# Kernel tuning notes

Measured on AMD Instinct MI355X. Metric: run time of the kernel, lower is better.

Reference implementation:

```python
import jax, jax.numpy as jnp
import numpy as np

C_IN, C_OUT, N, H, W = 128, 256, 3, 256, 256


def im2row(x, n, h, w, c):
    """x: [h*w, c] channel-last pixel-major image -> [(h-n+1)*(w-n+1), c*n*n]
    with each row ordered (channel, ki, kj) to match w.reshape(C_OUT,-1).T."""
    img = x.reshape(h, w, c)
    oh, ow = h - n + 1, w - n + 1
    # stack the n*n shifted views; last axis index = ki*n + kj
    patches = jnp.stack(
        [img[ki:ki + oh, kj:kj + ow, :] for ki in range(n) for kj in range(n)],
        axis=-1,
    )  # [oh, ow, c, n*n]
    return patches.reshape(oh * ow, c * n * n)


def setup_inputs() -> dict:
    key = jax.random.key(0)
    k1, k2, k3, k4 = jax.random.split(key, 4)
    x = jax.random.normal(k1, (H * W, C_IN), dtype=jnp.float32)
    # pre-quantized int8 kernel values (stored as int32), symmetric range
    kernel_q = jax.random.randint(k2, (C_IN * N * N, C_OUT), -127, 128, dtype=jnp.int32)
    kernel_scale = jax.random.uniform(k3, (1,), dtype=jnp.float32, minval=1e-3, maxval=1e-2)
    bias = jax.random.normal(k4, (C_OUT,), dtype=jnp.float32)
    return {"x": x, "kernel_q": kernel_q, "kernel_scale": kernel_scale, "bias": bias}


def reference(x, kernel_q, kernel_scale, bias):
    # im2row unfolding (irregular gather)
    rows = im2row(x, N, H, W, C_IN)                      # [OH*OW, C_IN*N*N]
    # int8 quantized matmul (weights dequantized by per-tensor scale) + bias
    acc = rows @ kernel_q.astype(jnp.float32)            # [OH*OW, C_OUT]
    return acc * kernel_scale + bias
```

## Files before the change

### kernel.cpp

```cpp
#include <hip/hip_runtime.h>
#include <hip/hip_bf16.h>
#include <stdint.h>

#define HH 256
#define WW 256
#define CIN 128
#define COUT 256
#define OHW 64516
#define KTOT 1152

#define BM 128
#define BN 256
#define BK 64
#define NSTEP 18

typedef __attribute__((ext_vector_type(8))) short short8;
typedef __attribute__((ext_vector_type(4))) float float4v;
typedef __attribute__((ext_vector_type(4))) float f32x4;

__device__ __forceinline__ short f2bf(float f) {
    unsigned u = __builtin_bit_cast(unsigned, f);
    unsigned r = u + 0x7fffu + ((u >> 16) & 1u);
    return (short)(r >> 16);
}

__device__ __forceinline__ short8 cvt8(float4v a, float4v b) {
    short8 r;
    r[0] = f2bf(a[0]); r[1] = f2bf(a[1]); r[2] = f2bf(a[2]); r[3] = f2bf(a[3]);
    r[4] = f2bf(b[0]); r[5] = f2bf(b[1]); r[6] = f2bf(b[2]); r[7] = f2bf(b[3]);
    return r;
}

__global__ void prep_weights(const int* __restrict__ kq, unsigned short* __restrict__ wt) {
    int tid = blockIdx.x * 256 + threadIdx.x;
    if (tid >= KTOT * COUT) return;
    int k  = tid >> 8;
    int co = tid & 255;
    int c  = k / 9;
    int q  = k - c * 9;
    int kp = q * 128 + c;
    wt[co * KTOT + kp] = (unsigned short)f2bf((float)kq[tid]);
}

__global__ __launch_bounds__(512, 2) void conv_gemm(
    const float* __restrict__ x,
    const unsigned short* __restrict__ wt,
    const float* __restrict__ scale_p,
    const float* __restrict__ bias,
    float* __restrict__ out)
{
    __shared__ __align__(16) char lds[BM * BK * 2 + BN * BK * 2];
    char* asb = lds;
    char* bsb = lds + BM * BK * 2;

    const int tid   = threadIdx.x;
    const int pbase = blockIdx.x * BM;

    const int arow = tid >> 2;
    const int asub = tid & 3;
    int p = pbase + arow;
    if (p > OHW - 1) p = OHW - 1;
    const int oy = p / 254;
    const int ox = p - oy * 254;
    const float* xrow = x + (oy * WW + ox) * CIN + asub * 16;

    const int bco  = tid >> 1;
    const int bsub = tid & 1;
    const unsigned short* wrow = wt + bco * KTOT + bsub * 32;

    const int lane = tid & 63;
    const int wid  = tid >> 6;
    const int wr   = wid >> 2;
    const int wc   = wid & 3;
    const int lhi  = lane >> 4;
    const int llo  = lane & 15;

    f32x4 acc[4][4];
#pragma unroll
    for (int m = 0; m < 4; m++)
#pragma unroll
        for (int n = 0; n < 4; n++) acc[m][n] = (f32x4)0.f;

    for (int tk = 0; tk < NSTEP; ++tk) {
        const int q  = tk >> 1;
        const int c0 = (tk & 1) << 6;
        const int ki = q / 3;
        const int kj = q - ki * 3;

        const float* src = xrow + (ki * WW + kj) * CIN + c0;
        float4v va0 = *(const float4v*)(src + 0);
        float4v va1 = *(const float4v*)(src + 4);
        float4v va2 = *(const float4v*)(src + 8);
        float4v va3 = *(const float4v*)(src + 12);

        const unsigned short* bsrc = wrow + tk * 64;
        short8 vb0 = *(const short8*)(bsrc + 0);
        short8 vb1 = *(const short8*)(bsrc + 8);
        short8 vb2 = *(const short8*)(bsrc + 16);
        short8 vb3 = *(const short8*)(bsrc + 24);

        __syncthreads();

        {
            short8 w0 = cvt8(va0, va1);
            short8 w1 = cvt8(va2, va3);
            int base = arow * 128 + asub * 32;
            int swz  = (arow & 7) << 4;
            *(short8*)(asb + ((base +  0) ^ swz)) = w0;
            *(short8*)(asb + ((base + 16) ^ swz)) = w1;
        }
        {
            int base = bco * 128 + bsub * 64;
            int swz  = (bco & 7) << 4;
            *(short8*)(bsb + ((base +  0) ^ swz)) = vb0;
            *(short8*)(bsb + ((base + 16) ^ swz)) = vb1;
            *(short8*)(bsb + ((base + 32) ^ swz)) = vb2;
            *(short8*)(bsb + ((base + 48) ^ swz)) = vb3;
        }

        __syncthreads();

#pragma unroll
        for (int kk = 0; kk < 2; ++kk) {
            short8 af[4], bfr[4];
#pragma unroll
            for (int m = 0; m < 4; m++) {
                int row  = wr * 64 + m * 16 + llo;
                int byte = row * 128 + kk * 64 + lhi * 16;
                byte ^= (row & 7) << 4;
                af[m] = *(const short8*)(asb + byte);
            }
#pragma unroll
            for (int n = 0; n < 4; n++) {
                int co   = wc * 64 + n * 16 + llo;
                int byte = co * 128 + kk * 64 + lhi * 16;
                byte ^= (co & 7) << 4;
                bfr[n] = *(const short8*)(bsb + byte);
            }
#pragma unroll
            for (int m = 0; m < 4; m++)
#pragma unroll
                for (int n = 0; n < 4; n++)
                    acc[m][n] = __builtin_amdgcn_mfma_f32_16x16x32_bf16(
                        af[m], bfr[n], acc[m][n], 0, 0, 0);
        }
    }

    const float scl = scale_p[0];
#pragma unroll
    for (int n = 0; n < 4; n++) {
        const int col = wc * 64 + n * 16 + llo;
        const float bv = bias[col];
#pragma unroll
        for (int m = 0; m < 4; m++) {
            const int prow = pbase + wr * 64 + m * 16 + lhi * 4;
#pragma unroll
            for (int r = 0; r < 4; r++) {
                const int pp = prow + r;
                if (pp < OHW)
                    out[pp * COUT + col] = acc[m][n][r] * scl + bv;
            }
        }
    }
}

extern "C" void kernel_launch(void* const* d_in, const int* in_sizes, int n_in,
                              void* d_out, int out_size, void* d_ws, size_t ws_size,
                              hipStream_t stream) {
    const float* x      = (const float*)d_in[0];
    const int*   kq     = (const int*)d_in[1];
    const float* scale  = (const float*)d_in[2];
    const float* bias   = (const float*)d_in[3];
    float*       out    = (float*)d_out;
    unsigned short* wt  = (unsigned short*)d_ws;

    prep_weights<<<KTOT, 256, 0, stream>>>(kq, wt);

    const int nblk = (OHW + BM - 1) / BM;
    conv_gemm<<<nblk, 512, 0, stream>>>(x, wt, scale, bias, out);
}
```

Measured before the change: 148.5 us.

## Double-buffer LDS with direct global-to-LDS weight loads and 256-row tiles

New measurement: 163.5 us. +10.1%, slower.

```diff
diff --git a/kernel.cpp b/kernel.cpp
--- a/kernel.cpp
+++ b/kernel.cpp
@@ -1,22 +1,21 @@
 #include <hip/hip_runtime.h>
-#include <hip/hip_bf16.h>
 #include <stdint.h>
 
-#define HH 256
 #define WW 256
 #define CIN 128
 #define COUT 256
 #define OHW 64516
 #define KTOT 1152
-
-#define BM 128
-#define BN 256
+#define BM 256
 #define BK 64
 #define NSTEP 18
+#define NWG 253
+#define BUFSZ 65536
 
 typedef __attribute__((ext_vector_type(8))) short short8;
 typedef __attribute__((ext_vector_type(4))) float float4v;
 typedef __attribute__((ext_vector_type(4))) float f32x4;
+typedef __attribute__((ext_vector_type(4))) unsigned int uint4v;
 
 __device__ __forceinline__ short f2bf(float f) {
     unsigned u = __builtin_bit_cast(unsigned, f);
@@ -24,23 +23,31 @@
     return (short)(r >> 16);
 }
 
-__device__ __forceinline__ short8 cvt8(float4v a, float4v b) {
-    short8 r;
-    r[0] = f2bf(a[0]); r[1] = f2bf(a[1]); r[2] = f2bf(a[2]); r[3] = f2bf(a[3]);
-    r[4] = f2bf(b[0]); r[5] = f2bf(b[1]); r[6] = f2bf(b[2]); r[7] = f2bf(b[3]);
+__global__ void prep_weights(const int* __restrict__ kq, unsigned short* __restrict__ wt) {
+    int o  = blockIdx.x * 256 + threadIdx.x;
+    int co = o / KTOT;
+    int kp = o - co * KTOT;
+    int q  = kp >> 7;
+    int c  = kp & 127;
+    wt[o] = (unsigned short)f2bf((float)kq[(c * 9 + q) * 256 + co]);
+}
+
+__device__ __forceinline__ void gload16(const void* g, void* l) {
+    __builtin_amdgcn_global_load_lds(
+        (const __attribute__((address_space(1))) unsigned int*)g,
+        (__attribute__((address_space(3))) unsigned int*)l, 16, 0, 0);
+}
+
+__device__ __forceinline__ unsigned cvtpk(float lo, float hi) {
+    unsigned r;
+    asm("v_cvt_pk_bf16_f32 %0, %1, %2" : "=v"(r) : "v"(lo), "v"(hi));
     return r;
 }
 
-__global__ void prep_weights(const int* __restrict__ kq, unsigned short* __restrict__ wt) {
-    int tid = blockIdx.x * 256 + threadIdx.x;
-    if (tid >= KTOT * COUT) return;
-    int k  = tid >> 8;
-    int co = tid & 255;
-    int c  = k / 9;
-    int q  = k - c * 9;
-    int kp = q * 128 + c;
-    wt[co * KTOT + kp] = (unsigned short)f2bf((float)kq[tid]);
-}
+#define SB  __builtin_amdgcn_sched_barrier(0)
+#define BAR __builtin_amdgcn_s_barrier()
+#define WAIT_VM(n) asm volatile("s_waitcnt vmcnt(" #n ")" ::: "memory")
+#define WAIT_LGKM  asm volatile("s_waitcnt lgkmcnt(0)" ::: "memory")
 
 __global__ __launch_bounds__(512, 2) void conv_gemm(
     const float* __restrict__ x,
@@ -49,133 +56,171 @@
     const float* __restrict__ bias,
     float* __restrict__ out)
 {
-    __shared__ __align__(16) char lds[BM * BK * 2 + BN * BK * 2];
-    char* asb = lds;
-    char* bsb = lds + BM * BK * 2;
-
-    const int tid   = threadIdx.x;
-    const int pbase = blockIdx.x * BM;
-
-    const int arow = tid >> 2;
-    const int asub = tid & 3;
+    __shared__ __align__(16) char lds[2 * BUFSZ];
+
+    const int tid  = threadIdx.x;
+    const int lane = tid & 63;
+    const int wave = tid >> 6;
+
+    const int orig = blockIdx.x;
+    const int xcd  = orig & 7;
+    const int idx8 = orig >> 3;
+    const int wg   = (xcd < 5 ? xcd * 32 : 160 + (xcd - 5) * 31) + idx8;
+    const int pbase = wg * BM;
+
+    const int arow  = tid >> 1;
+    const int ahalf = tid & 1;
+    {
+    }
     int p = pbase + arow;
     if (p > OHW - 1) p = OHW - 1;
     const int oy = p / 254;
     const int ox = p - oy * 254;
-    const float* xrow = x + (oy * WW + ox) * CIN + asub * 16;
-
-    const int bco  = tid >> 1;
-    const int bsub = tid & 1;
-    const unsigned short* wrow = wt + bco * KTOT + bsub * 32;
-
-    const int lane = tid & 63;
-    const int wid  = tid >> 6;
-    const int wr   = wid >> 2;
-    const int wc   = wid & 3;
-    const int lhi  = lane >> 4;
-    const int llo  = lane & 15;
-
-    f32x4 acc[4][4];
-#pragma unroll
-    for (int m = 0; m < 4; m++)
+    const float* abase = x + (oy * WW + ox) * CIN + ahalf * 32;
+    int adst[4];
+#pragma unroll
+    for (int jw = 0; jw < 4; ++jw)
+        adst[jw] = arow * 128 + ((ahalf * 64 + jw * 16) ^ ((arow & 7) << 4));
+
+    int bsrc[4];
+#pragma unroll
+    for (int it = 0; it < 4; ++it) {
+        int z    = it * 8192 + wave * 1024 + lane * 16;
+        int co   = z >> 7;
+        int colb = (z & 127) ^ ((co & 7) << 4);
+        bsrc[it] = co * KTOT + (colb >> 1);
+    }
+
+    const int wr128 = (wave >> 2) * 128;
+    const int wc64  = (wave & 3) * 64;
+    const int llo   = lane & 15;
+    const int lhi16 = (lane >> 4) * 16;
+
+    f32x4 acc[8][4];
+#pragma unroll
+    for (int m = 0; m < 8; m++)
 #pragma unroll
         for (int n = 0; n < 4; n++) acc[m][n] = (f32x4)0.f;
 
-    for (int tk = 0; tk < NSTEP; ++tk) {
-        const int q  = tk >> 1;
-        const int c0 = (tk & 1) << 6;
-        const int ki = q / 3;
-        const int kj = q - ki * 3;
-
-        const float* src = xrow + (ki * WW + kj) * CIN + c0;
-        float4v va0 = *(const float4v*)(src + 0);
-        float4v va1 = *(const float4v*)(src + 4);
-        float4v va2 = *(const float4v*)(src + 8);
-        float4v va3 = *(const float4v*)(src + 12);
-
-        const unsigned short* bsrc = wrow + tk * 64;
-        short8 vb0 = *(const short8*)(bsrc + 0);
-        short8 vb1 = *(const short8*)(bsrc + 8);
-        short8 vb2 = *(const short8*)(bsrc + 16);
-        short8 vb3 = *(const short8*)(bsrc + 24);
-
-        __syncthreads();
-
-        {
-            short8 w0 = cvt8(va0, va1);
-            short8 w1 = cvt8(va2, va3);
-            int base = arow * 128 + asub * 32;
-            int swz  = (arow & 7) << 4;
-            *(short8*)(asb + ((base +  0) ^ swz)) = w0;
-            *(short8*)(asb + ((base + 16) ^ swz)) = w1;
-        }
-        {
-            int base = bco * 128 + bsub * 64;
-            int swz  = (bco & 7) << 4;
-            *(short8*)(bsb + ((base +  0) ^ swz)) = vb0;
-            *(short8*)(bsb + ((base + 16) ^ swz)) = vb1;
-            *(short8*)(bsb + ((base + 32) ^ swz)) = vb2;
-            *(short8*)(bsb + ((base + 48) ^ swz)) = vb3;
-        }
-
-        __syncthreads();
-
-#pragma unroll
-        for (int kk = 0; kk < 2; ++kk) {
-            short8 af[4], bfr[4];
-#pragma unroll
-            for (int m = 0; m < 4; m++) {
-                int row  = wr * 64 + m * 16 + llo;
-                int byte = row * 128 + kk * 64 + lhi * 16;
-                byte ^= (row & 7) << 4;
-                af[m] = *(const short8*)(asb + byte);
-            }
-#pragma unroll
-            for (int n = 0; n < 4; n++) {
-                int co   = wc * 64 + n * 16 + llo;
-                int byte = co * 128 + kk * 64 + lhi * 16;
-                byte ^= (co & 7) << 4;
-                bfr[n] = *(const short8*)(bsb + byte);
-            }
-#pragma unroll
-            for (int m = 0; m < 4; m++)
-#pragma unroll
-                for (int n = 0; n < 4; n++)
-                    acc[m][n] = __builtin_amdgcn_mfma_f32_16x16x32_bf16(
-                        af[m], bfr[n], acc[m][n], 0, 0, 0);
-        }
-    }
+    float4v fr[8];
+
+#define ISSUE_A(tk) do {                                                        \
+    int q_ = (tk) >> 1;  int ki_ = q_ / 3;  int kj_ = q_ - ki_ * 3;             \
+    const float* asrc = abase + (ki_ * WW + kj_) * CIN + (((tk) & 1) << 6);     \
+    _Pragma("unroll")                                                           \
+    for (int j = 0; j < 8; ++j) fr[j] = ((const float4v*)asrc)[j];              \
+} while (0)
+
+#define WRITE_A(bufb) do {                                                      \
+    _Pragma("unroll")                                                           \
+    for (int jw = 0; jw < 4; ++jw) {                                            \
+        uint4v U;                                                               \
+        U.x = cvtpk(fr[2*jw][0], fr[2*jw][1]);                                  \
+        U.y = cvtpk(fr[2*jw][2], fr[2*jw][3]);                                  \
+        U.z = cvtpk(fr[2*jw+1][0], fr[2*jw+1][1]);                              \
+        U.w = cvtpk(fr[2*jw+1][2], fr[2*jw+1][3]);                              \
+        *(uint4v*)(lds + (bufb) + adst[jw]) = U;                                \
+    }                                                                           \
+} while (0)
+
+#define GLOAD_B(bufb, tk) do {                                                  \
+    _Pragma("unroll")                                                           \
+    for (int it = 0; it < 4; ++it)                                              \
+        gload16(wt + bsrc[it] + (tk) * 64,                                      \
+                lds + (bufb) + 32768 + it * 8192 + wave * 1024);                \
+} while (0)
+
+#define COMPUTE(bufb) do {                                                      \
+    _Pragma("unroll")                                                           \
+    for (int kk = 0; kk < 2; ++kk) {                                            \
+        short8 bfr[4];                                                          \
+        _Pragma("unroll")                                                       \
+        for (int n = 0; n < 4; ++n) {                                           \
+            int co  = wc64 + n * 16 + llo;                                      \
+            int off = co * 128 + ((kk * 64 + lhi16) ^ ((co & 7) << 4));         \
+            bfr[n] = *(const short8*)(lds + (bufb) + 32768 + off);              \
+        }                                                                       \
+        _Pragma("unroll")                                                       \
+        for (int mh = 0; mh < 2; ++mh) {                                        \
+            short8 af[4];                                                       \
+            _Pragma("unroll")                                                   \
+            for (int mi = 0; mi < 4; ++mi) {                                    \
+                int row = wr128 + mh * 64 + mi * 16 + llo;                      \
+                int off = row * 128 + ((kk * 64 + lhi16) ^ ((row & 7) << 4));   \
+                af[mi] = *(const short8*)(lds + (bufb) + off);                  \
+            }                                                                   \
+            __builtin_amdgcn_s_setprio(1);                                      \
+            _Pragma("unroll")                                                   \
+            for (int mi = 0; mi < 4; ++mi)                                      \
+                _Pragma("unroll")                                               \
+                for (int n = 0; n < 4; ++n)                                     \
+                    acc[mh * 4 + mi][n] = __builtin_amdgcn_mfma_f32_16x16x32_bf16( \
+                        af[mi], bfr[n], acc[mh * 4 + mi][n], 0, 0, 0);          \
+            __builtin_amdgcn_s_setprio(0);                                      \
+        }                                                                       \
+    }                                                                           \
+} while (0)
+
+    ISSUE_A(0);
+    GLOAD_B(0, 0);
+    SB; WAIT_VM(4); SB;
+    WRITE_A(0);
+    ISSUE_A(1);
+    GLOAD_B(BUFSZ, 1);
+    SB; WAIT_VM(12); SB;
+    WAIT_LGKM; SB; BAR; SB;
+
+#pragma unroll 2
+    for (int t = 0; t < NSTEP - 2; ++t) {
+        const int cur = (t & 1) * BUFSZ;
+        const int nxt = cur ^ BUFSZ;
+        WRITE_A(nxt);
+        COMPUTE(cur);
+        WAIT_LGKM; SB; BAR; SB;
+        ISSUE_A(t + 2);
+        GLOAD_B(cur, t + 2);
+        SB; WAIT_VM(12); SB;
+        BAR; SB;
+    }
+    WRITE_A(BUFSZ);
+    COMPUTE(0);
+    WAIT_LGKM; SB; BAR; SB;
+    WAIT_VM(0); SB; BAR; SB;
+    COMPUTE(BUFSZ);
 
     const float scl = scale_p[0];
-#pragma unroll
-    for (int n = 0; n < 4; n++) {
-        const int col = wc * 64 + n * 16 + llo;
+    const int lhi4 = (lane >> 4) * 4;
+#pragma unroll
+    for (int n = 0; n < 4; ++n) {
+        const int col = wc64 + n * 16 + llo;
         const float bv = bias[col];
 #pragma unroll
-        for (int m = 0; m < 4; m++) {
-            const int prow = pbase + wr * 64 + m * 16 + lhi * 4;
-#pragma unroll
-            for (int r = 0; r < 4; r++) {
+        for (int m = 0; m < 8; ++m) {
+            const int prow = pbase + wr128 + m * 16 + lhi4;
+#pragma unroll
+            for (int r = 0; r < 4; ++r) {
                 const int pp = prow + r;
                 if (pp < OHW)
                     out[pp * COUT + col] = acc[m][n][r] * scl + bv;
             }
         }
     }
+#undef ISSUE_A
+#undef WRITE_A
+#undef GLOAD_B
+#undef COMPUTE
 }
 
 extern "C" void kernel_launch(void* const* d_in, const int* in_sizes, int n_in,
                               void* d_out, int out_size, void* d_ws, size_t ws_size,
                               hipStream_t stream) {
-    const float* x      = (const float*)d_in[0];
-    const int*   kq     = (const int*)d_in[1];
-    const float* scale  = (const float*)d_in[2];
-    const float* bias   = (const float*)d_in[3];
-    float*       out    = (float*)d_out;
-    unsigned short* wt  = (unsigned short*)d_ws;
+    const float* x     = (const float*)d_in[0];
+    const int*   kq    = (const int*)d_in[1];
+    const float* scale = (const float*)d_in[2];
+    const float* bias  = (const float*)d_in[3];
+    float*       out   = (float*)d_out;
+    unsigned short* wt = (unsigned short*)d_ws;
 
     prep_weights<<<KTOT, 256, 0, stream>>>(kq, wt);
-
-    const int nblk = (OHW + BM - 1) / BM;
-    conv_gemm<<<nblk, 512, 0, stream>>>(x, wt, scale, bias, out);
-}
+    conv_gemm<<<NWG, 512, 0, stream>>>(x, wt, scale, bias, out);
+}
```
